# Performance work log

Hardware: AMD Instinct MI355X
Metric: run time of the kernel (lower is better)

Reference implementation:

```python
import jax, jax.numpy as jnp
import numpy as np

B, N, E = 4, 2048, 512
H, DK, DV = 8, 64, 64
QKV_OUT = H * (2 * DK + DV)  # 1536


def setup_inputs() -> dict:
    key = jax.random.key(0)
    ks = jax.random.split(key, 5)
    s_in = 1.0 / np.sqrt(E)
    s_o = 1.0 / np.sqrt(H * DV)
    x = jax.random.normal(ks[0], (B, N, E), dtype=jnp.float32)
    W_qkv = jax.random.uniform(ks[1], (E, QKV_OUT), jnp.float32, -s_in, s_in)
    b_qkv = jax.random.uniform(ks[2], (QKV_OUT,), jnp.float32, -s_in, s_in)
    W_o = jax.random.uniform(ks[3], (H * DV, E), jnp.float32, -s_o, s_o)
    b_o = jax.random.uniform(ks[4], (E,), jnp.float32, -s_o, s_o)
    return {"x": x, "W_qkv": W_qkv, "b_qkv": b_qkv, "W_o": W_o, "b_o": b_o}


def reference(x, W_qkv, b_qkv, W_o, b_o):
    scale = DK ** (-0.5)
    qkv = x @ W_qkv + b_qkv                      # [B, N, H*(2dk+dv)]
    # Faithful to torch: raw view (B, H, N, 2dk+dv), NOT a head-split transpose.
    qkv = qkv.reshape(B, H, N, 2 * DK + DV)
    q = qkv[..., :DK]
    k = qkv[..., DK:2 * DK]
    v = qkv[..., 2 * DK:]
    # Faithful bug: qk /= scale with scale = dk^-0.5 -> multiply by sqrt(dk).
    qk = jnp.einsum('bhnd,bhmd->bhnm', q, k) / scale   # [B, H, N, N]
    attn = jax.nn.softmax(qk, axis=-1)
    y = jnp.einsum('bhnm,bhmd->bhnd', attn, v)         # [B, H, N, dv]
    y = y.reshape(B, N, H * DV)
    return y @ W_o + b_o
```

## Files before the change

kernel.cpp:

```cpp
#include <hip/hip_runtime.h>
#include <hip/hip_bf16.h>
#include <math.h>


typedef __attribute__((ext_vector_type(8))) short bf16x8;
typedef __attribute__((ext_vector_type(4))) float f32x4;

#define MFMA16(a, b, c) __builtin_amdgcn_mfma_f32_16x16x32_bf16((a), (b), (c), 0, 0, 0)

__device__ __forceinline__ ushort f2bf_rne(float f) {
  union { float f; unsigned u; } v; v.f = f;
  return (ushort)((v.u + 0x7fffu + ((v.u >> 16) & 1u)) >> 16);
}
__device__ __forceinline__ float bf2f(ushort h) {
  union { float f; unsigned u; } v; v.u = ((unsigned)h) << 16; return v.f;
}
__device__ __forceinline__ void split2(float f, ushort& hi, ushort& lo) {
  union { float f; unsigned u; } v; v.f = f;
  hi = (ushort)(v.u >> 16);
  union { float f; unsigned u; } r; r.f = f - bf2f(hi);
  lo = (ushort)(r.u >> 16);
}

typedef __attribute__((address_space(3))) unsigned int lds_uint;
typedef const __attribute__((address_space(1))) unsigned int glob_uint;
__device__ __forceinline__ void gl_lds16(const ushort* g, short* l) {
  __builtin_amdgcn_global_load_lds((glob_uint*)g, (lds_uint*)l, 16, 0, 0);
}

template <bool ROOMY>
__global__ __launch_bounds__(256) void cvt_k(const float* __restrict__ wqkv,
                                             const float* __restrict__ wo,
                                             const float* __restrict__ x,
                                             ushort* __restrict__ wT_hi,
                                             ushort* __restrict__ wT_lo,
                                             ushort* __restrict__ woT,
                                             ushort* __restrict__ xh,
                                             ushort* __restrict__ xl)
{
  const int gid = blockIdx.x * 256 + threadIdx.x;
  if (gid < 786432) {
    const int c   = gid / 49152;
    const int rem = gid - c * 49152;
    const int n   = rem >> 5;
    const int k   = c * 32 + (rem & 31);
    ushort hi, lo; split2(wqkv[(size_t)k * 1536 + n], hi, lo);
    wT_hi[gid] = hi; wT_lo[gid] = lo;
  } else if (gid < 1048576) {
    const int g = gid - 786432;
    const int n = g >> 9, k = g & 511;
    woT[g] = f2bf_rne(wo[(size_t)k * 512 + n]);
  } else if (ROOMY) {
    const int g = gid - 1048576;
    float4 v = ((const float4*)x)[g];
    ushort4 hh, ll;
    split2(v.x, hh.x, ll.x); split2(v.y, hh.y, ll.y);
    split2(v.z, hh.z, ll.z); split2(v.w, hh.w, ll.w);
    ((ushort4*)xh)[g] = hh;
    ((ushort4*)xl)[g] = ll;
  }
}

template <bool PRECVT>
__global__ __launch_bounds__(256) void qkv_gemm_k(
    const float* __restrict__ x,
    const ushort* __restrict__ xh, const ushort* __restrict__ xl,
    const ushort* __restrict__ wT_hi, const ushort* __restrict__ wT_lo,
    const float* __restrict__ bqkv,
    ushort* __restrict__ q_hi, ushort* __restrict__ q_lo,
    ushort* __restrict__ k_hi, ushort* __restrict__ k_lo,
    ushort* __restrict__ v_nat)
{
  const int i = blockIdx.x, j = i >> 3;
  const int tmb = (i & 7) * 8 + (j & 7);
  const int tn  = j >> 3;
  const int tid = threadIdx.x, lane = tid & 63, w = tid >> 6;
  const int col16 = lane & 15, quad = lane >> 4;
  const int wr = w >> 1, wc = w & 1;

  __shared__ short sbuf[16384];

  const int wl   = w * 1024 + lane * 8;
  const int ldsw = w * 1024;
  const ushort* shp = wT_hi + (size_t)tn * 4096 + wl;
  const ushort* slp = wT_lo + (size_t)tn * 4096 + wl;

  const float*  axf[4];
  const ushort *axh[4], *axl[4];
#pragma unroll
  for (int rt = 0; rt < 4; ++rt) {
    const size_t rowoff = (size_t)(tmb * 128 + wr * 64 + rt * 16 + col16) * 512 + quad * 8;
    axf[rt] = x  + rowoff;
    axh[rt] = xh + rowoff;
    axl[rt] = xl + rowoff;
  }

  f32x4 acc[4][4];
#pragma unroll
  for (int rt = 0; rt < 4; ++rt)
#pragma unroll
    for (int ct = 0; ct < 4; ++ct) acc[rt][ct] = (f32x4){0.f, 0.f, 0.f, 0.f};

  gl_lds16(shp,       sbuf + ldsw);
  gl_lds16(shp + 512, sbuf + ldsw + 512);
  gl_lds16(slp,       sbuf + 8192 + ldsw);
  gl_lds16(slp + 512, sbuf + 8192 + ldsw + 512);
  __syncthreads();

  int buf = 0;
#pragma unroll
  for (int c = 0; c < 16; ++c) {
    if (c < 15) {
      const size_t co = (size_t)(c + 1) * 49152;
      const int nb = (buf ^ 1) * 4096;
      gl_lds16(shp + co,       sbuf + nb + ldsw);
      gl_lds16(shp + co + 512, sbuf + nb + ldsw + 512);
      gl_lds16(slp + co,       sbuf + 8192 + nb + ldsw);
      gl_lds16(slp + co + 512, sbuf + 8192 + nb + ldsw + 512);
    }
    const int k0 = c * 32;
    const short* bhb = sbuf + buf * 4096;
    const short* blb = sbuf + 8192 + buf * 4096;

    bf16x8 bh[4], bl[4];
#pragma unroll
    for (int ct = 0; ct < 4; ++ct) {
      const int roff = (wc * 64 + ct * 16 + col16) * 32 + quad * 8;
      bh[ct] = *(const bf16x8*)(bhb + roff);
      bl[ct] = *(const bf16x8*)(blb + roff);
    }
#pragma unroll
    for (int rt = 0; rt < 4; ++rt) {
      bf16x8 a_hi, a_lo;
      if constexpr (PRECVT) {
        a_hi = *(const bf16x8*)(axh[rt] + k0);
        a_lo = *(const bf16x8*)(axl[rt] + k0);
      } else {
        float4 xa = *(const float4*)(axf[rt] + k0);
        float4 xb = *(const float4*)(axf[rt] + k0 + 4);
#pragma unroll
        for (int jj = 0; jj < 4; ++jj) {
          ushort h, l;
          split2(((const float*)&xa)[jj], h, l);
          ((short*)&a_hi)[jj] = (short)h; ((short*)&a_lo)[jj] = (short)l;
          split2(((const float*)&xb)[jj], h, l);
          ((short*)&a_hi)[4 + jj] = (short)h; ((short*)&a_lo)[4 + jj] = (short)l;
        }
      }
#pragma unroll
      for (int ct = 0; ct < 4; ++ct) {
        acc[rt][ct] = MFMA16(a_hi, bh[ct], acc[rt][ct]);
        acc[rt][ct] = MFMA16(a_hi, bl[ct], acc[rt][ct]);
        acc[rt][ct] = MFMA16(a_lo, bh[ct], acc[rt][ct]);
      }
    }
    __syncthreads();
    buf ^= 1;
  }

  short* eph = sbuf + w * 2304;
  short* epl = eph + 1152;
  const int g0   = tn * 128 + wc * 64;
  const int sect = (g0 % 192) >> 6;
  const int s    = g0 / 192;
  float bv[4];
#pragma unroll
  for (int ct = 0; ct < 4; ++ct) bv[ct] = bqkv[g0 + ct * 16 + col16];

#pragma unroll
  for (int rt = 0; rt < 4; ++rt) {
#pragma unroll
    for (int ct = 0; ct < 4; ++ct) {
#pragma unroll
      for (int r = 0; r < 4; ++r) {
        const float val = acc[rt][ct][r] + bv[ct];
        const int o = (quad * 4 + r) * 72 + ct * 16 + col16;
        if (sect == 2) {
          eph[o] = (short)f2bf_rne(val);
        } else {
          ushort h, l; split2(val, h, l);
          eph[o] = (short)h; epl[o] = (short)l;
        }
      }
    }
#pragma unroll
    for (int p = 0; p < 2; ++p) {
      const int row = p * 8 + (lane >> 3);
      const int dsg = (lane & 7) * 8;
      const int grow = tmb * 128 + wr * 64 + rt * 16 + row;
      const int bhh = grow >> 8, a = grow & 255;
      const size_t idx = ((size_t)bhh * 2048 + 8 * a + s) * 64 + dsg;
      uint4 hv = *(const uint4*)(eph + row * 72 + dsg);
      if (sect == 0) {
        *(uint4*)(q_hi + idx) = hv;
        uint4 lv = *(const uint4*)(epl + row * 72 + dsg);
        *(uint4*)(q_lo + idx) = lv;
      } else if (sect == 1) {
        *(uint4*)(k_hi + idx) = hv;
        uint4 lv = *(const uint4*)(epl + row * 72 + dsg);
        *(uint4*)(k_lo + idx) = lv;
      } else {
        *(uint4*)(v_nat + idx) = hv;
      }
    }
  }
}

__global__ __launch_bounds__(256) void vtrans_k(const ushort* __restrict__ v_nat,
                                                ushort* __restrict__ vT)
{
  const int t  = blockIdx.x & 7;
  const int bh = blockIdx.x >> 3;
  const int tid = threadIdx.x;
  const int nl = tid & 63;
  const int dg = tid >> 6;
  const size_t base = (size_t)bh * 2048 * 64;
#pragma unroll
  for (int p = 0; p < 2; ++p) {
    const int dseg = dg + p * 4;
#pragma unroll
    for (int nb = 0; nb < 4; ++nb) {
      const int n = t * 256 + nb * 64 + nl;
      uint4 vv = *(const uint4*)(v_nat + base + (size_t)n * 64 + dseg * 8);
      const ushort* pv = (const ushort*)&vv;
#pragma unroll
      for (int j = 0; j < 8; ++j)
        vT[base + (size_t)(dseg * 8 + j) * 2048 + n] = pv[j];
    }
  }
}

__global__ __launch_bounds__(256, 2) void attn_k(
    const ushort* __restrict__ q_hi, const ushort* __restrict__ q_lo,
    const ushort* __restrict__ k_hi, const ushort* __restrict__ k_lo,
    const ushort* __restrict__ vT, ushort* __restrict__ y)
{
  const int i  = blockIdx.x;
  const int bh = (i & 7) * 4 + (i >> 7);
  const int qt = (i >> 3) & 15;
  const int tid = threadIdx.x, lane = tid & 63, w = tid >> 6;
  const int col16 = lane & 15, quad = lane >> 4;

  __shared__ short kh_lds[2][64][72], kl_lds[2][64][72], vt_lds[2][64][72];
  __shared__ short p_lds[4][2][16][72];

  const size_t base = (size_t)bh * 2048 * 64;
  const int qw = qt * 128 + w * 32;

  bf16x8 qh[2][2], ql[2][2];
#pragma unroll
  for (int rf = 0; rf < 2; ++rf)
#pragma unroll
    for (int ks = 0; ks < 2; ++ks) {
      const size_t off = base + (size_t)(qw + rf * 16 + col16) * 64 + ks * 32 + quad * 8;
      qh[rf][ks] = *(const bf16x8*)(q_hi + off);
      ql[rf][ks] = *(const bf16x8*)(q_lo + off);
    }

  f32x4 oacc[2][4];
#pragma unroll
  for (int rf = 0; rf < 2; ++rf)
#pragma unroll
    for (int ct = 0; ct < 4; ++ct) oacc[rf][ct] = (f32x4){0.f, 0.f, 0.f, 0.f};
  f32x4 lsum[2] = {(f32x4){0.f, 0.f, 0.f, 0.f}, (f32x4){0.f, 0.f, 0.f, 0.f}};

  const int sn = tid >> 2, sd = (tid & 3) * 16;
  const ushort* khsrc = k_hi + base + (size_t)sn * 64 + sd;
  const ushort* klsrc = k_lo + base + (size_t)sn * 64 + sd;
  const ushort* vtsrc = vT  + base + (size_t)sn * 2048 + sd;

  const float S2 = 11.541560327111707f;

  uint4 r0 = *(const uint4*)(khsrc);
  uint4 r1 = *(const uint4*)(khsrc + 8);
  uint4 r2 = *(const uint4*)(klsrc);
  uint4 r3 = *(const uint4*)(klsrc + 8);
  uint4 r4 = *(const uint4*)(vtsrc);
  uint4 r5 = *(const uint4*)(vtsrc + 8);
  *(uint4*)(&kh_lds[0][sn][sd])     = r0;
  *(uint4*)(&kh_lds[0][sn][sd + 8]) = r1;
  *(uint4*)(&kl_lds[0][sn][sd])     = r2;
  *(uint4*)(&kl_lds[0][sn][sd + 8]) = r3;
  *(uint4*)(&vt_lds[0][sn][sd])     = r4;
  *(uint4*)(&vt_lds[0][sn][sd + 8]) = r5;

  for (int c = 0; c < 32; ++c) {
    __syncthreads();
    if (c < 31) {
      const size_t ko = (size_t)(c + 1) * 4096;
      r0 = *(const uint4*)(khsrc + ko);
      r1 = *(const uint4*)(khsrc + ko + 8);
      r2 = *(const uint4*)(klsrc + ko);
      r3 = *(const uint4*)(klsrc + ko + 8);
      r4 = *(const uint4*)(vtsrc + (c + 1) * 64);
      r5 = *(const uint4*)(vtsrc + (c + 1) * 64 + 8);
    }
    const int b = c & 1;

    f32x4 sacc[2][4];
#pragma unroll
    for (int rf = 0; rf < 2; ++rf)
#pragma unroll
      for (int ct = 0; ct < 4; ++ct) sacc[rf][ct] = (f32x4){0.f, 0.f, 0.f, 0.f};
#pragma unroll
    for (int ks = 0; ks < 2; ++ks) {
#pragma unroll
      for (int ct = 0; ct < 4; ++ct) {
        bf16x8 khf = *(const bf16x8*)(&kh_lds[b][ct * 16 + col16][ks * 32 + quad * 8]);
        bf16x8 klf = *(const bf16x8*)(&kl_lds[b][ct * 16 + col16][ks * 32 + quad * 8]);
#pragma unroll
        for (int rf = 0; rf < 2; ++rf) {
          sacc[rf][ct] = MFMA16(qh[rf][ks], khf, sacc[rf][ct]);
          sacc[rf][ct] = MFMA16(qh[rf][ks], klf, sacc[rf][ct]);
          sacc[rf][ct] = MFMA16(ql[rf][ks], khf, sacc[rf][ct]);
        }
      }
    }

#pragma unroll
    for (int rf = 0; rf < 2; ++rf) {
#pragma unroll
      for (int ct = 0; ct < 4; ++ct) {
#pragma unroll
        for (int r = 0; r < 4; ++r) {
          const float p = __builtin_amdgcn_exp2f(fmaf(sacc[rf][ct][r], S2, -128.0f));
          union { float f; unsigned u; } pu; pu.f = p;
          union { unsigned u; float f; } pb; pb.u = pu.u & 0xffff0000u;
          lsum[rf][r] += pb.f;
          p_lds[w][rf][quad * 4 + r][ct * 16 + col16] = (short)(pu.u >> 16);
        }
      }
    }

#pragma unroll
    for (int ks = 0; ks < 2; ++ks) {
#pragma unroll
      for (int ct = 0; ct < 4; ++ct) {
        bf16x8 vv = *(const bf16x8*)(&vt_lds[b][ct * 16 + col16][ks * 32 + quad * 8]);
#pragma unroll
        for (int rf = 0; rf < 2; ++rf) {
          bf16x8 ap = *(const bf16x8*)(&p_lds[w][rf][col16][ks * 32 + quad * 8]);
          oacc[rf][ct] = MFMA16(ap, vv, oacc[rf][ct]);
        }
      }
    }

    if (c < 31) {
      const int nb = b ^ 1;
      *(uint4*)(&kh_lds[nb][sn][sd])     = r0;
      *(uint4*)(&kh_lds[nb][sn][sd + 8]) = r1;
      *(uint4*)(&kl_lds[nb][sn][sd])     = r2;
      *(uint4*)(&kl_lds[nb][sn][sd + 8]) = r3;
      *(uint4*)(&vt_lds[nb][sn][sd])     = r4;
      *(uint4*)(&vt_lds[nb][sn][sd + 8]) = r5;
    }
  }

#pragma unroll
  for (int rf = 0; rf < 2; ++rf) {
#pragma unroll
    for (int r = 0; r < 4; ++r) {
      float l = lsum[rf][r];
#pragma unroll
      for (int off = 1; off < 16; off <<= 1) l += __shfl_xor(l, off, 64);
      const float inv = 1.f / l;
      const int n = qw + rf * 16 + quad * 4 + r;
      const size_t orow = ((size_t)bh * 256 + (n >> 3)) * 512 + (n & 7) * 64;
#pragma unroll
      for (int ct = 0; ct < 4; ++ct)
        y[orow + ct * 16 + col16] = f2bf_rne(oacc[rf][ct][r] * inv);
    }
  }
}

__global__ __launch_bounds__(256) void out_gemm_k(
    const ushort* __restrict__ y, const ushort* __restrict__ woT,
    const float* __restrict__ bo, float* __restrict__ out)
{
  const int i = blockIdx.x, j = i >> 3;
  const int tmb = (i & 7) * 32 + (j & 31);
  const int tn  = j >> 5;
  const int tid = threadIdx.x, lane = tid & 63, w = tid >> 6;
  const int col16 = lane & 15, quad = lane >> 4;
  const int wr = w >> 1, wc = w & 1;

  __shared__ short b_lds[2][128][40];

  const int sn = tid >> 1, sk = (tid & 1) * 16;
  const ushort* bsrc = woT + (size_t)(tn * 128 + sn) * 512 + sk;

  const ushort* ay = y + (size_t)(tmb * 32 + wr * 16 + col16) * 512 + quad * 8;

  f32x4 acc[4];
#pragma unroll
  for (int ct = 0; ct < 4; ++ct) acc[ct] = (f32x4){0.f, 0.f, 0.f, 0.f};

  uint4 rb0 = *(const uint4*)(bsrc);
  uint4 rb1 = *(const uint4*)(bsrc + 8);
  *(uint4*)(&b_lds[0][sn][sk])     = rb0;
  *(uint4*)(&b_lds[0][sn][sk + 8]) = rb1;

  for (int c = 0; c < 16; ++c) {
    __syncthreads();
    if (c < 15) {
      const int k0 = (c + 1) * 32;
      rb0 = *(const uint4*)(bsrc + k0);
      rb1 = *(const uint4*)(bsrc + k0 + 8);
    }
    const int b = c & 1, k0 = c * 32;
    bf16x8 af = *(const bf16x8*)(ay + k0);
#pragma unroll
    for (int ct = 0; ct < 4; ++ct) {
      bf16x8 bfr = *(const bf16x8*)(&b_lds[b][wc * 64 + ct * 16 + col16][quad * 8]);
      acc[ct] = MFMA16(af, bfr, acc[ct]);
    }
    if (c < 15) {
      const int nb = b ^ 1;
      *(uint4*)(&b_lds[nb][sn][sk])     = rb0;
      *(uint4*)(&b_lds[nb][sn][sk + 8]) = rb1;
    }
  }
#pragma unroll
  for (int ct = 0; ct < 4; ++ct) {
    const int col = tn * 128 + wc * 64 + ct * 16 + col16;
    const float bval = bo[col];
#pragma unroll
    for (int r = 0; r < 4; ++r) {
      const int row = tmb * 32 + wr * 16 + quad * 4 + r;
      out[(size_t)row * 512 + col] = acc[ct][r] + bval;
    }
  }
}

extern "C" void kernel_launch(void* const* d_in, const int* in_sizes, int n_in,
                              void* d_out, int out_size, void* d_ws, size_t ws_size,
                              hipStream_t stream)
{
  const float* x    = (const float*)d_in[0];
  const float* Wqkv = (const float*)d_in[1];
  const float* bqkv = (const float*)d_in[2];
  const float* Wo   = (const float*)d_in[3];
  const float* bo   = (const float*)d_in[4];
  float* out = (float*)d_out;

  ushort* wT_hi = (ushort*)d_ws;
  ushort* wT_lo = wT_hi + 786432;
  ushort* woT   = wT_lo + 786432;
  ushort* q_hi  = woT   + 262144;
  ushort* q_lo  = q_hi  + 4194304;
  ushort* k_hi  = q_lo  + 4194304;
  ushort* k_lo  = k_hi  + 4194304;
  ushort* v_nat = k_lo  + 4194304;
  ushort* tail  = v_nat + 4194304;

  const bool roomy = ws_size >= 62390272ULL;
  ushort *xh, *xl, *vT, *y;
  if (roomy) {
    xh = tail; xl = tail + 4194304;
    vT = xh;   y  = xl;
  } else {
    xh = xl = nullptr;
    vT = tail; y = v_nat;
  }

  if (roomy) {
    cvt_k<true><<<8192, 256, 0, stream>>>(Wqkv, Wo, x, wT_hi, wT_lo, woT, xh, xl);
    qkv_gemm_k<true><<<768, 256, 0, stream>>>(x, xh, xl, wT_hi, wT_lo, bqkv,
                                              q_hi, q_lo, k_hi, k_lo, v_nat);
  } else {
    cvt_k<false><<<4096, 256, 0, stream>>>(Wqkv, Wo, x, wT_hi, wT_lo, woT,
                                           nullptr, nullptr);
    qkv_gemm_k<false><<<768, 256, 0, stream>>>(x, nullptr, nullptr, wT_hi, wT_lo,
                                               bqkv, q_hi, q_lo, k_hi, k_lo, v_nat);
  }
  vtrans_k<<<256, 256, 0, stream>>>(v_nat, vT);
  attn_k<<<512, 256, 0, stream>>>(q_hi, q_lo, k_hi, k_lo, vT, y);
  out_gemm_k<<<1024, 256, 0, stream>>>(y, woT, bo, out);
}
```

Baseline: 231.5 us.

## Stage attention K/V tiles with direct global-to-LDS loads and XOR-swizzled layout

Replaces the register-staged double buffering of K-hi, K-lo and V-transposed tiles in the attention kernel with direct global-to-LDS copies (gl_lds16) into one unified shared buffer. The shared buffer uses an XOR swizzle on 8-element segments, for the K/V planes and the per-wave P tile alike, in place of padded rows. Instruction priority is also raised around the MFMA loops. The aim is to cut VGPR pressure and LDS bank conflicts and to overlap the next chunk's load with compute. The risks are the correctness of the swizzle indexing and the wait semantics of the async LDS loads around the single barrier.

```diff
diff --git a/kernel.cpp b/kernel.cpp
--- a/kernel.cpp
+++ b/kernel.cpp
@@ -240,12 +240,19 @@
   const int qt = (i >> 3) & 15;
   const int tid = threadIdx.x, lane = tid & 63, w = tid >> 6;
   const int col16 = lane & 15, quad = lane >> 4;
-
-  __shared__ short kh_lds[2][64][72], kl_lds[2][64][72], vt_lds[2][64][72];
-  __shared__ short p_lds[4][2][16][72];
+  const int n7 = col16 & 7;
+
+  __shared__ short sbuf[32768];
 
   const size_t base = (size_t)bh * 2048 * 64;
   const int qw = qt * 128 + w * 32;
+
+  const ushort* khs = k_hi + base;
+  const ushort* kls = k_lo + base;
+  const ushort* vts = vT  + base;
+
+  const int lrow = lane >> 3;
+  const int lx8  = ((lane & 7) ^ lrow) * 8;
 
   bf16x8 qh[2][2], ql[2][2];
 #pragma unroll
@@ -264,50 +271,51 @@
     for (int ct = 0; ct < 4; ++ct) oacc[rf][ct] = (f32x4){0.f, 0.f, 0.f, 0.f};
   f32x4 lsum[2] = {(f32x4){0.f, 0.f, 0.f, 0.f}, (f32x4){0.f, 0.f, 0.f, 0.f}};
 
-  const int sn = tid >> 2, sd = (tid & 3) * 16;
-  const ushort* khsrc = k_hi + base + (size_t)sn * 64 + sd;
-  const ushort* klsrc = k_lo + base + (size_t)sn * 64 + sd;
-  const ushort* vtsrc = vT  + base + (size_t)sn * 2048 + sd;
-
   const float S2 = 11.541560327111707f;
 
-  uint4 r0 = *(const uint4*)(khsrc);
-  uint4 r1 = *(const uint4*)(khsrc + 8);
-  uint4 r2 = *(const uint4*)(klsrc);
-  uint4 r3 = *(const uint4*)(klsrc + 8);
-  uint4 r4 = *(const uint4*)(vtsrc);
-  uint4 r5 = *(const uint4*)(vtsrc + 8);
-  *(uint4*)(&kh_lds[0][sn][sd])     = r0;
-  *(uint4*)(&kh_lds[0][sn][sd + 8]) = r1;
-  *(uint4*)(&kl_lds[0][sn][sd])     = r2;
-  *(uint4*)(&kl_lds[0][sn][sd + 8]) = r3;
-  *(uint4*)(&vt_lds[0][sn][sd])     = r4;
-  *(uint4*)(&vt_lds[0][sn][sd + 8]) = r5;
-
+  short* wp0 = sbuf + 24576 + w * 2048;
+
+#define STAGE_CHUNK(cnext, nb)                                                \
+  {                                                                           \
+    _Pragma("unroll")                                                         \
+    for (int ii = 0; ii < 6; ++ii) {                                          \
+      const int ins = w * 6 + ii;                                             \
+      const int plane = ins >> 3, sub = ins & 7;                              \
+      short* dst = sbuf + ((nb) * 3 + plane) * 4096 + sub * 512;              \
+      const ushort* src;                                                      \
+      if (plane == 2)                                                         \
+        src = vts + (size_t)(sub * 8 + lrow) * 2048 + (cnext) * 64 + lx8;     \
+      else                                                                    \
+        src = (plane ? kls : khs) + (cnext) * 4096 + sub * 512 + lrow * 64 + lx8; \
+      gl_lds16(src, dst);                                                     \
+    }                                                                         \
+  }
+
+  STAGE_CHUNK(0, 0);
+  __syncthreads();
+
+  int buf = 0;
   for (int c = 0; c < 32; ++c) {
-    __syncthreads();
-    if (c < 31) {
-      const size_t ko = (size_t)(c + 1) * 4096;
-      r0 = *(const uint4*)(khsrc + ko);
-      r1 = *(const uint4*)(khsrc + ko + 8);
-      r2 = *(const uint4*)(klsrc + ko);
-      r3 = *(const uint4*)(klsrc + ko + 8);
-      r4 = *(const uint4*)(vtsrc + (c + 1) * 64);
-      r5 = *(const uint4*)(vtsrc + (c + 1) * 64 + 8);
-    }
-    const int b = c & 1;
+    if (c < 31) STAGE_CHUNK(c + 1, buf ^ 1);
+
+    const short* kb = sbuf + (buf * 3) * 4096;
+    const short* lb = kb + 4096;
+    const short* vb = kb + 8192;
 
     f32x4 sacc[2][4];
 #pragma unroll
     for (int rf = 0; rf < 2; ++rf)
 #pragma unroll
       for (int ct = 0; ct < 4; ++ct) sacc[rf][ct] = (f32x4){0.f, 0.f, 0.f, 0.f};
+
+    __builtin_amdgcn_s_setprio(1);
 #pragma unroll
     for (int ks = 0; ks < 2; ++ks) {
 #pragma unroll
       for (int ct = 0; ct < 4; ++ct) {
-        bf16x8 khf = *(const bf16x8*)(&kh_lds[b][ct * 16 + col16][ks * 32 + quad * 8]);
-        bf16x8 klf = *(const bf16x8*)(&kl_lds[b][ct * 16 + col16][ks * 32 + quad * 8]);
+        const int off = (ct * 16 + col16) * 64 + (((ks * 4 + quad) ^ n7) << 3);
+        bf16x8 khf = *(const bf16x8*)(kb + off);
+        bf16x8 klf = *(const bf16x8*)(lb + off);
 #pragma unroll
         for (int rf = 0; rf < 2; ++rf) {
           sacc[rf][ct] = MFMA16(qh[rf][ks], khf, sacc[rf][ct]);
@@ -316,6 +324,7 @@
         }
       }
     }
+    __builtin_amdgcn_s_setprio(0);
 
 #pragma unroll
     for (int rf = 0; rf < 2; ++rf) {
@@ -327,33 +336,32 @@
           union { float f; unsigned u; } pu; pu.f = p;
           union { unsigned u; float f; } pb; pb.u = pu.u & 0xffff0000u;
           lsum[rf][r] += pb.f;
-          p_lds[w][rf][quad * 4 + r][ct * 16 + col16] = (short)(pu.u >> 16);
+          const int prow = quad * 4 + r;
+          wp0[rf * 1024 + prow * 64 + ((ct * 16 + col16) ^ ((prow & 7) << 3))] =
+              (short)(pu.u >> 16);
         }
       }
     }
 
+    __builtin_amdgcn_s_setprio(1);
 #pragma unroll
     for (int ks = 0; ks < 2; ++ks) {
 #pragma unroll
       for (int ct = 0; ct < 4; ++ct) {
-        bf16x8 vv = *(const bf16x8*)(&vt_lds[b][ct * 16 + col16][ks * 32 + quad * 8]);
+        const int voff = (ct * 16 + col16) * 64 + (((ks * 4 + quad) ^ n7) << 3);
+        bf16x8 vv = *(const bf16x8*)(vb + voff);
+        const int poff = col16 * 64 + (((ks * 4 + quad) ^ n7) << 3);
 #pragma unroll
         for (int rf = 0; rf < 2; ++rf) {
-          bf16x8 ap = *(const bf16x8*)(&p_lds[w][rf][col16][ks * 32 + quad * 8]);
+          bf16x8 ap = *(const bf16x8*)(wp0 + rf * 1024 + poff);
           oacc[rf][ct] = MFMA16(ap, vv, oacc[rf][ct]);
         }
       }
     }
-
-    if (c < 31) {
-      const int nb = b ^ 1;
-      *(uint4*)(&kh_lds[nb][sn][sd])     = r0;
-      *(uint4*)(&kh_lds[nb][sn][sd + 8]) = r1;
-      *(uint4*)(&kl_lds[nb][sn][sd])     = r2;
-      *(uint4*)(&kl_lds[nb][sn][sd + 8]) = r3;
-      *(uint4*)(&vt_lds[nb][sn][sd])     = r4;
-      *(uint4*)(&vt_lds[nb][sn][sd + 8]) = r5;
-    }
+    __builtin_amdgcn_s_setprio(0);
+
+    __syncthreads();
+    buf ^= 1;
   }
 
 #pragma unroll
@@ -371,6 +379,7 @@
         y[orow + ct * 16 + col16] = f2bf_rne(oacc[rf][ct][r] * inv);
     }
   }
+#undef STAGE_CHUNK
 }
 
 __global__ __launch_bounds__(256) void out_gemm_k(
```

Result: no change. 231.4 us (-0.1%).
